# Kernel optimization log

Measured on AMD Instinct MI355X. Metric: run time of the kernel, lower is better.

## Reference

```python
import jax, jax.numpy as jnp
import numpy as np


def setup_inputs() -> dict:
    key = jax.random.key(0)
    k1, k2 = jax.random.split(key)
    support_features = jax.random.normal(k1, (1000, 5, 512), dtype=jnp.float32)
    query_features = jax.random.normal(k2, (5000, 512), dtype=jnp.float32)
    return {"support_features": support_features, "query_features": query_features, "use_cosine": 1}


def reference(support_features, query_features, use_cosine):
    # Preprocess: mean-center over (classes, shots), then L2-normalize per vector.
    mean = jnp.mean(support_features, axis=(0, 1), keepdims=True)  # [1,1,D]
    s = support_features - mean                                    # [C,S,D]
    q = query_features - mean[0]                                   # [Q,D]
    s = s / jnp.linalg.norm(s, axis=2, keepdims=True)
    q = q / jnp.linalg.norm(q, axis=1, keepdims=True)
    if use_cosine:
        # cosine sims without materializing [C,Q,S,D]; einsum fuses the dot.
        sims = jnp.einsum('csd,qd->cqs', s, q)   # [C,Q,S]
        best = jnp.max(sims, axis=2)             # [C,Q] best shot per class
        return jnp.argmax(best, axis=0)          # [Q] predicted class
    else:
        # euclidean cdist(query[Q,D], support[C,S,D]) -> [C,Q,S]
        d2 = (jnp.sum(q * q, axis=1)[None, :, None]
              + jnp.sum(s * s, axis=2)[:, None, :]
              - 2.0 * jnp.einsum('csd,qd->cqs', s, q))
        dist = jnp.sqrt(jnp.maximum(d2, 0.0))
        best = jnp.min(dist, axis=2)
        return jnp.argmin(best, axis=0)
```

## Files before the change

kernel.cpp:

```cpp
#include <hip/hip_runtime.h>
#include <stdint.h>

#define D     512
#define NSUP  5000
#define NQRY  5000
#define NPAD  5120
#define MEAN_BLOCKS 100
#define ROWS_PER_MEAN_BLOCK 50
#define SCALE 512.0f

#define OFF_SHI     0
#define OFF_SLO     5242880
#define OFF_QHI     10485760
#define OFF_QLO     15728640
#define OFF_PARTIAL 20971520
#define OFF_MEAN    21176320
#define OFF_KEYS    21178368

#define SH_SHI   0
#define SH_SLO   32768
#define SH_QHI   65536
#define SH_QLO   98304
#define SH_KL    131072
#define SH_TOTAL (131072 + 2048)

typedef _Float16 half4v __attribute__((ext_vector_type(4)));
typedef _Float16 half8v __attribute__((ext_vector_type(8)));
typedef float    f32x4  __attribute__((ext_vector_type(4)));

__device__ __forceinline__ unsigned long long pack_key(float v, int sidx) {
    unsigned u = __float_as_uint(v);
    u = (u & 0x80000000u) ? ~u : (u | 0x80000000u);
    return ((unsigned long long)u << 32) | (unsigned)(0xFFFFFFFFu - (unsigned)sidx);
}

__device__ __forceinline__ void gload16(const void* g, void* l) {
    __builtin_amdgcn_global_load_lds(
        (const __attribute__((address_space(1))) unsigned int*)g,
        (__attribute__((address_space(3))) unsigned int*)l, 16, 0, 0);
}

__global__ void k_partial_mean(const float* __restrict__ sup, float* __restrict__ partial) {
    const int col = threadIdx.x;
    const int b   = blockIdx.x;
    const int r0  = b * ROWS_PER_MEAN_BLOCK;
    float acc = 0.0f;
    #pragma unroll 5
    for (int r = 0; r < ROWS_PER_MEAN_BLOCK; ++r)
        acc += sup[(size_t)(r0 + r) * D + col];
    partial[b * D + col] = acc;
}

__global__ void k_mean_init(const float* __restrict__ partial, float* __restrict__ mean,
                            unsigned long long* __restrict__ keys) {
    const int col = threadIdx.x;
    float acc = 0.0f;
    #pragma unroll 4
    for (int b = 0; b < MEAN_BLOCKS; ++b) acc += partial[b * D + col];
    mean[col] = acc * (1.0f / (float)NSUP);
    for (int i = col; i < NSUP; i += 512) keys[i] = 0ull;
}

__global__ void k_split(const float* __restrict__ sup, const float* __restrict__ qry,
                        const float* __restrict__ mean,
                        _Float16* __restrict__ shi, _Float16* __restrict__ slo,
                        _Float16* __restrict__ qhi, _Float16* __restrict__ qlo) {
    const int t    = threadIdx.x;
    const int rloc = t >> 7;
    const int tc   = t & 127;
    const int b    = (int)blockIdx.x * 4 + rloc;
    const float* src; _Float16 *dhi, *dlo; int valid;
    if (b < NPAD) { src = sup + (size_t)b * D;
                    dhi = shi + (size_t)b * D; dlo = slo + (size_t)b * D; valid = (b < NSUP); }
    else          { int r = b - NPAD; src = qry + (size_t)r * D;
                    dhi = qhi + (size_t)r * D; dlo = qlo + (size_t)r * D; valid = (r < NQRY); }
    __shared__ float red[8];
    if (!valid) {
        half4v z = {};
        *(half4v*)(dhi + tc * 4) = z;
        *(half4v*)(dlo + tc * 4) = z;
        return;
    }
    float4 v = *(const float4*)(src + tc * 4);
    float4 m = *(const float4*)(mean + tc * 4);
    v.x -= m.x; v.y -= m.y; v.z -= m.z; v.w -= m.w;
    float ss = v.x * v.x + v.y * v.y + v.z * v.z + v.w * v.w;
    #pragma unroll
    for (int off = 32; off > 0; off >>= 1) ss += __shfl_down(ss, off, 64);
    if ((t & 63) == 0) red[t >> 6] = ss;
    __syncthreads();
    const float rn = SCALE / sqrtf(red[rloc * 2] + red[rloc * 2 + 1]);
    float sv[4] = {v.x * rn, v.y * rn, v.z * rn, v.w * rn};
    half4v h, l;
    #pragma unroll
    for (int i = 0; i < 4; ++i) {
        _Float16 hh = (_Float16)sv[i];
        h[i] = hh;
        l[i] = (_Float16)(sv[i] - (float)hh);
    }
    *(half4v*)(dhi + tc * 4) = h;
    *(half4v*)(dlo + tc * 4) = l;
}

__launch_bounds__(512, 2)
__global__ void k_main(const _Float16* __restrict__ shi, const _Float16* __restrict__ slo,
                       const _Float16* __restrict__ qhi, const _Float16* __restrict__ qlo,
                       unsigned long long* __restrict__ keys) {
    extern __shared__ char smem[];
    char* lshi = smem + SH_SHI;
    char* lslo = smem + SH_SLO;
    char* lqhi = smem + SH_QHI;
    char* lqlo = smem + SH_QLO;
    unsigned long long* kl = (unsigned long long*)(smem + SH_KL);

    const int tid  = threadIdx.x;
    const int lane = tid & 63;
    const int wv   = tid >> 6;
    const int q0   = blockIdx.x * 256;
    const int s0   = blockIdx.y * 256;
    const int wr   = wv >> 2;
    const int wc   = wv & 3;

    if (tid < 256) kl[tid] = 0ull;

    const int srow = wv * 16 + (lane >> 2);
    const int sl0  = ((lane & 3) ^ ((lane >> 3) & 3)) * 16;
    const size_t gA0 = (size_t)(s0 + srow) * 1024 + sl0;
    const size_t gB0 = (size_t)(q0 + srow) * 1024 + sl0;
    const char* pShi = (const char*)shi; const char* pSlo = (const char*)slo;
    const char* pQhi = (const char*)qhi; const char* pQlo = (const char*)qlo;
    const int dst0 = wv * 1024;
    const int dst1 = 8192 + wv * 1024;

    const int l15 = lane & 15;
    const int kg  = lane >> 4;
    const int swz = (kg ^ ((l15 >> 1) & 3)) * 16;
    const int foA = (wr * 128 + l15) * 64 + swz;
    const int foB = (wc * 64  + l15) * 64 + swz;

    f32x4 acc[8][4] = {};

#define BAR()    asm volatile("s_barrier" ::: "memory")
#define WAITV8() asm volatile("s_waitcnt vmcnt(8)" ::: "memory")
#define WAITV0() asm volatile("s_waitcnt vmcnt(0)" ::: "memory")
#define WAITL()  asm volatile("s_waitcnt lgkmcnt(0)" ::: "memory")

#define STAGE(P, KT) do {                                                   \
        const size_t kb_ = (size_t)(KT) * 64;                               \
        gload16(pShi + gA0 + kb_,          lshi + (P) * 16384 + dst0);      \
        gload16(pShi + gA0 + 131072 + kb_, lshi + (P) * 16384 + dst1);      \
        gload16(pSlo + gA0 + kb_,          lslo + (P) * 16384 + dst0);      \
        gload16(pSlo + gA0 + 131072 + kb_, lslo + (P) * 16384 + dst1);      \
        gload16(pQhi + gB0 + kb_,          lqhi + (P) * 16384 + dst0);      \
        gload16(pQhi + gB0 + 131072 + kb_, lqhi + (P) * 16384 + dst1);      \
        gload16(pQlo + gB0 + kb_,          lqlo + (P) * 16384 + dst0);      \
        gload16(pQlo + gB0 + 131072 + kb_, lqlo + (P) * 16384 + dst1);      \
    } while (0)

#define RD_A(P, QA) do { _Pragma("unroll")                                  \
        for (int i_ = 0; i_ < 4; ++i_) {                                    \
            ah[i_] = *(const half8v*)(lshi + (P)*16384 + foA + ((QA)*4 + i_)*1024); \
            al[i_] = *(const half8v*)(lslo + (P)*16384 + foA + ((QA)*4 + i_)*1024); \
        } } while (0)

#define RD_B(P, QB) do { _Pragma("unroll")                                  \
        for (int j_ = 0; j_ < 2; ++j_) {                                    \
            bh[j_] = *(const half8v*)(lqhi + (P)*16384 + foB + ((QB)*2 + j_)*1024); \
            bl[j_] = *(const half8v*)(lqlo + (P)*16384 + foB + ((QB)*2 + j_)*1024); \
        } } while (0)

#define MMA(QA, QB) do {                                                    \
        __builtin_amdgcn_s_setprio(1);                                      \
        _Pragma("unroll")                                                   \
        for (int i_ = 0; i_ < 4; ++i_)                                      \
        { _Pragma("unroll")                                                 \
          for (int j_ = 0; j_ < 2; ++j_) {                                  \
            f32x4* a_ = &acc[(QA)*4 + i_][(QB)*2 + j_];                     \
            *a_ = __builtin_amdgcn_mfma_f32_16x16x32_f16(ah[i_], bh[j_], *a_, 0, 0, 0); \
            *a_ = __builtin_amdgcn_mfma_f32_16x16x32_f16(ah[i_], bl[j_], *a_, 0, 0, 0); \
            *a_ = __builtin_amdgcn_mfma_f32_16x16x32_f16(al[i_], bh[j_], *a_, 0, 0, 0); \
          } }                                                               \
        __builtin_amdgcn_s_setprio(0);                                      \
        __builtin_amdgcn_sched_barrier(0);                                  \
    } while (0)

#define COMPUTE_TILE(P) do {                                                \
        half8v ah[4], al[4], bh[2], bl[2];                                  \
        RD_A(P, 0); RD_B(P, 0); MMA(0, 0);                                  \
        RD_B(P, 1);             MMA(0, 1);                                  \
        RD_A(P, 1); RD_B(P, 0); MMA(1, 0);                                  \
        RD_B(P, 1);             MMA(1, 1);                                  \
    } while (0)

#define HALF(P, TT) do {                                                    \
        COMPUTE_TILE(P);                                                    \
        WAITL(); BAR();                       \
        if ((TT) + 2 < 16) { STAGE(P, (TT) + 2); WAITV8(); }                \
        else               { WAITV0(); }                                    \
        BAR();                                \
    } while (0)

    STAGE(0, 0);
    STAGE(1, 1);
    WAITV8();
    BAR();

    for (int t = 0; t < 16; t += 2) {
        HALF(0, t);
        HALF(1, t + 1);
    }

#undef HALF
#undef COMPUTE_TILE
#undef MMA
#undef RD_B
#undef RD_A
#undef STAGE

    #pragma unroll
    for (int fb = 0; fb < 4; ++fb) {
        unsigned long long best = 0ull;
        #pragma unroll
        for (int fa = 0; fa < 8; ++fa)
            #pragma unroll
            for (int r = 0; r < 4; ++r) {
                const int s = s0 + wr * 128 + fa * 16 + kg * 4 + r;
                if (s < NSUP) {
                    unsigned long long k = pack_key(acc[fa][fb][r], s);
                    if (k > best) best = k;
                }
            }
        unsigned long long o = __shfl_xor(best, 16, 64); if (o > best) best = o;
        o = __shfl_xor(best, 32, 64);                    if (o > best) best = o;
        if (kg == 0) atomicMax(&kl[wc * 64 + fb * 16 + l15], best);
    }
    __syncthreads();
    if (tid < 256) {
        const int q = q0 + tid;
        if (q < NQRY && kl[tid] != 0ull) atomicMax(&keys[q], kl[tid]);
    }
}

__global__ void k_decode(const unsigned long long* __restrict__ keys, int* __restrict__ out) {
    const int q = blockIdx.x * 256 + threadIdx.x;
    if (q < NQRY) {
        unsigned sidx = 0xFFFFFFFFu - (unsigned)(keys[q] & 0xFFFFFFFFull);
        out[q] = (int)(sidx / 5u);
    }
}

extern "C" void kernel_launch(void* const* d_in, const int* in_sizes, int n_in,
                              void* d_out, int out_size, void* d_ws, size_t ws_size,
                              hipStream_t stream) {
    const float* sup = (const float*)d_in[0];
    const float* qry = (const float*)d_in[1];
    int* out = (int*)d_out;

    char* ws = (char*)d_ws;
    _Float16* shi = (_Float16*)(ws + OFF_SHI);
    _Float16* slo = (_Float16*)(ws + OFF_SLO);
    _Float16* qhi = (_Float16*)(ws + OFF_QHI);
    _Float16* qlo = (_Float16*)(ws + OFF_QLO);
    float* partial = (float*)(ws + OFF_PARTIAL);
    float* mean    = (float*)(ws + OFF_MEAN);
    unsigned long long* keys = (unsigned long long*)(ws + OFF_KEYS);

    static bool attr_set = false;
    if (!attr_set) {
        (void)hipFuncSetAttribute((const void*)k_main,
                                  hipFuncAttributeMaxDynamicSharedMemorySize, SH_TOTAL);
        attr_set = true;
    }

    k_partial_mean<<<MEAN_BLOCKS, 512, 0, stream>>>(sup, partial);
    k_mean_init<<<1, 512, 0, stream>>>(partial, mean, keys);
    k_split<<<(2 * NPAD) / 4, 512, 0, stream>>>(sup, qry, mean, shi, slo, qhi, qlo);
    dim3 grid(NPAD / 256, NPAD / 256);
    k_main<<<grid, 512, SH_TOTAL, stream>>>(shi, slo, qhi, qlo, keys);
    k_decode<<<(NQRY + 255) / 256, 256, 0, stream>>>(keys, out);
}
```

Baseline: 174.7 us.

## Interleave next-tile global prefetch with MFMA phases, keep B fragments in registers

Replaces the two-half, two-tiles-ahead double-buffer loop with a single-tile-ahead schedule. The staging loads for the next K tile are split into three groups, each issued between LDS reads and an MFMA quadrant, with barriers around each MFMA block. B fragments are held in two register sets so the second A half reuses them instead of re-reading LDS. This aims to spread global-load issue across compute and cut redundant LDS reads, at the cost of extra barriers, higher register pressure, and a shallower prefetch distance that waits for all loads each iteration.

```diff
diff --git a/kernel.cpp b/kernel.cpp
--- a/kernel.cpp
+++ b/kernel.cpp
@@ -141,18 +141,20 @@
     f32x4 acc[8][4] = {};
 
 #define BAR()    asm volatile("s_barrier" ::: "memory")
-#define WAITV8() asm volatile("s_waitcnt vmcnt(8)" ::: "memory")
 #define WAITV0() asm volatile("s_waitcnt vmcnt(0)" ::: "memory")
 #define WAITL()  asm volatile("s_waitcnt lgkmcnt(0)" ::: "memory")
 
-#define STAGE(P, KT) do {                                                   \
-        const size_t kb_ = (size_t)(KT) * 64;                               \
+#define STAGE_A(P, KT) do { const size_t kb_ = (size_t)(KT) * 64;           \
         gload16(pShi + gA0 + kb_,          lshi + (P) * 16384 + dst0);      \
         gload16(pShi + gA0 + 131072 + kb_, lshi + (P) * 16384 + dst1);      \
         gload16(pSlo + gA0 + kb_,          lslo + (P) * 16384 + dst0);      \
+    } while (0)
+#define STAGE_B(P, KT) do { const size_t kb_ = (size_t)(KT) * 64;           \
         gload16(pSlo + gA0 + 131072 + kb_, lslo + (P) * 16384 + dst1);      \
         gload16(pQhi + gB0 + kb_,          lqhi + (P) * 16384 + dst0);      \
         gload16(pQhi + gB0 + 131072 + kb_, lqhi + (P) * 16384 + dst1);      \
+    } while (0)
+#define STAGE_C(P, KT) do { const size_t kb_ = (size_t)(KT) * 64;           \
         gload16(pQlo + gB0 + kb_,          lqlo + (P) * 16384 + dst0);      \
         gload16(pQlo + gB0 + 131072 + kb_, lqlo + (P) * 16384 + dst1);      \
     } while (0)
@@ -163,59 +165,68 @@
             al[i_] = *(const half8v*)(lslo + (P)*16384 + foA + ((QA)*4 + i_)*1024); \
         } } while (0)
 
-#define RD_B(P, QB) do { _Pragma("unroll")                                  \
+#define RD_B(P, QB, BH, BL) do { _Pragma("unroll")                          \
         for (int j_ = 0; j_ < 2; ++j_) {                                    \
-            bh[j_] = *(const half8v*)(lqhi + (P)*16384 + foB + ((QB)*2 + j_)*1024); \
-            bl[j_] = *(const half8v*)(lqlo + (P)*16384 + foB + ((QB)*2 + j_)*1024); \
+            BH[j_] = *(const half8v*)(lqhi + (P)*16384 + foB + ((QB)*2 + j_)*1024); \
+            BL[j_] = *(const half8v*)(lqlo + (P)*16384 + foB + ((QB)*2 + j_)*1024); \
         } } while (0)
 
-#define MMA(QA, QB) do {                                                    \
+#define MMA_Q(QA, QB, BH, BL) do {                                          \
         __builtin_amdgcn_s_setprio(1);                                      \
         _Pragma("unroll")                                                   \
         for (int i_ = 0; i_ < 4; ++i_)                                      \
         { _Pragma("unroll")                                                 \
           for (int j_ = 0; j_ < 2; ++j_) {                                  \
             f32x4* a_ = &acc[(QA)*4 + i_][(QB)*2 + j_];                     \
-            *a_ = __builtin_amdgcn_mfma_f32_16x16x32_f16(ah[i_], bh[j_], *a_, 0, 0, 0); \
-            *a_ = __builtin_amdgcn_mfma_f32_16x16x32_f16(ah[i_], bl[j_], *a_, 0, 0, 0); \
-            *a_ = __builtin_amdgcn_mfma_f32_16x16x32_f16(al[i_], bh[j_], *a_, 0, 0, 0); \
+            *a_ = __builtin_amdgcn_mfma_f32_16x16x32_f16(ah[i_], BH[j_], *a_, 0, 0, 0); \
+            *a_ = __builtin_amdgcn_mfma_f32_16x16x32_f16(ah[i_], BL[j_], *a_, 0, 0, 0); \
+            *a_ = __builtin_amdgcn_mfma_f32_16x16x32_f16(al[i_], BH[j_], *a_, 0, 0, 0); \
           } }                                                               \
         __builtin_amdgcn_s_setprio(0);                                      \
         __builtin_amdgcn_sched_barrier(0);                                  \
     } while (0)
 
-#define COMPUTE_TILE(P) do {                                                \
-        half8v ah[4], al[4], bh[2], bl[2];                                  \
-        RD_A(P, 0); RD_B(P, 0); MMA(0, 0);                                  \
-        RD_B(P, 1);             MMA(0, 1);                                  \
-        RD_A(P, 1); RD_B(P, 0); MMA(1, 0);                                  \
-        RD_B(P, 1);             MMA(1, 1);                                  \
-    } while (0)
-
-#define HALF(P, TT) do {                                                    \
-        COMPUTE_TILE(P);                                                    \
-        WAITL(); BAR();                       \
-        if ((TT) + 2 < 16) { STAGE(P, (TT) + 2); WAITV8(); }                \
-        else               { WAITV0(); }                                    \
-        BAR();                                \
-    } while (0)
-
-    STAGE(0, 0);
-    STAGE(1, 1);
-    WAITV8();
+    STAGE_A(0, 0); STAGE_B(0, 0); STAGE_C(0, 0);
+    WAITV0();
     BAR();
 
-    for (int t = 0; t < 16; t += 2) {
-        HALF(0, t);
-        HALF(1, t + 1);
-    }
-
-#undef HALF
-#undef COMPUTE_TILE
-#undef MMA
+    for (int t = 0; t < 16; ++t) {
+        const int P    = t & 1;
+        const int Pn   = P ^ 1;
+        const int n    = t + 1;
+        const bool more = (n < 16);
+        half8v ah[4], al[4], bh0[2], bl0[2], bh1[2], bl1[2];
+
+        RD_A(P, 0);
+        RD_B(P, 0, bh0, bl0);
+        if (more) STAGE_A(Pn, n);
+        BAR(); WAITL();
+        MMA_Q(0, 0, bh0, bl0);
+        BAR();
+
+        RD_B(P, 1, bh1, bl1);
+        if (more) STAGE_B(Pn, n);
+        BAR(); WAITL();
+        MMA_Q(0, 1, bh1, bl1);
+        BAR();
+
+        RD_A(P, 1);
+        if (more) STAGE_C(Pn, n);
+        BAR(); WAITL();
+        MMA_Q(1, 0, bh0, bl0);
+        BAR();
+
+        MMA_Q(1, 1, bh1, bl1);
+        WAITV0();
+        BAR();
+    }
+
+#undef MMA_Q
 #undef RD_B
 #undef RD_A
-#undef STAGE
+#undef STAGE_C
+#undef STAGE_B
+#undef STAGE_A
 
     #pragma unroll
     for (int fb = 0; fb < 4; ++fb) {
```

New measurement: 165.7 us. 5.2% less time.
